# Optimization experiments

Measured on AMD Instinct MI355X. Metric: run time of the kernel, lower is better.

## Reference

```python
import jax, jax.numpy as jnp
import numpy as np

B, N, E, H, HID = 4, 2048, 1024, 16, 4096
D = E // H
EPS = 1e-5


def setup_inputs() -> dict:
    key = jax.random.key(0)
    ks = jax.random.split(key, 8)
    s = 0.02
    return {
        "x": jax.random.normal(ks[0], (B, N, E), dtype=jnp.float32),
        "Wqkv": jax.random.normal(ks[1], (3 * E, E), dtype=jnp.float32) * s,
        "bqkv": jnp.zeros((3 * E,), dtype=jnp.float32),
        "Wo": jax.random.normal(ks[2], (E, E), dtype=jnp.float32) * s,
        "bo": jnp.zeros((E,), dtype=jnp.float32),
        "ln1_g": jnp.ones((E,), dtype=jnp.float32),
        "ln1_b": jnp.zeros((E,), dtype=jnp.float32),
        "W1": jax.random.normal(ks[3], (HID, E), dtype=jnp.float32) * s,
        "bf1": jnp.zeros((HID,), dtype=jnp.float32),
        "W2": jax.random.normal(ks[4], (E, HID), dtype=jnp.float32) * s,
        "bf2": jnp.zeros((E,), dtype=jnp.float32),
        "ln2_g": jnp.ones((E,), dtype=jnp.float32),
        "ln2_b": jnp.zeros((E,), dtype=jnp.float32),
    }


def _layernorm(x, g, b):
    m = jnp.mean(x, axis=-1, keepdims=True)
    v = jnp.mean(jnp.square(x - m), axis=-1, keepdims=True)
    return (x - m) * jax.lax.rsqrt(v + EPS) * g + b


def reference(x, Wqkv, bqkv, Wo, bo, ln1_g, ln1_b, W1, bf1, W2, bf2, ln2_g, ln2_b):
    Bx, Nx, Ex = x.shape
    # --- MultiHeadSelfAttention (faithful to original, including its einsum-label quirk) ---
    qkv = x @ Wqkv.T + bqkv                                   # (B,N,3E)
    qkv = qkv.reshape(Bx, Nx, 3, H, D).transpose(2, 0, 3, 1, 4)  # (3,B,H,N,D)
    q, k, v = qkv[0], qkv[1], qkv[2]                          # each (B,H,N,D)
    # original torch labels: q/k interpreted as (n,q,h,d) -> energy (B,N,H,H)
    energy = jnp.einsum('nqhd,nkhd->nhqk', q, k)
    attention = jax.nn.softmax(energy / (Ex ** 0.5), axis=-1)  # softmax over heads axis
    out = jnp.einsum('nhql,nlhd->nqhd', attention, v).reshape(Bx, Nx, Ex)
    attn_out = out @ Wo.T + bo
    # --- residual + LN1 ---
    h = _layernorm(x + attn_out, ln1_g, ln1_b)
    # --- FFN (dropout is identity in eval) ---
    f = jax.nn.gelu(h @ W1.T + bf1, approximate=False) @ W2.T + bf2
    # --- residual + LN2 ---
    return _layernorm(h + f, ln2_g, ln2_b)
```

## Files before the change

### kernel.cpp

```cpp
#include <hip/hip_runtime.h>
#include <hip/hip_bf16.h>
#include <math.h>

typedef __hip_bfloat16 bf16;
typedef __bf16 bf8v __attribute__((ext_vector_type(8)));
typedef float f4v __attribute__((ext_vector_type(4)));

__device__ inline float gelu_act(float v) {
    return 0.5f * v * (1.f + erff(v * 0.70710678118654752f));
}

__device__ inline void gld16(const void* g, void* l) {
    __builtin_amdgcn_global_load_lds(
        (__attribute__((address_space(1))) void*)g,
        (__attribute__((address_space(3))) void*)l, 16, 0, 0);
}

__global__ __launch_bounds__(256)
void cast_f2b(const float* __restrict__ X, bf16* __restrict__ Y, long n)
{
    const long i = ((long)blockIdx.x * 256 + threadIdx.x) * 4;
    if (i + 3 < n) {
        const float4 v = *(const float4*)(X + i);
        Y[i + 0] = __float2bfloat16(v.x);
        Y[i + 1] = __float2bfloat16(v.y);
        Y[i + 2] = __float2bfloat16(v.z);
        Y[i + 3] = __float2bfloat16(v.w);
    }
}

template<int ACT, bool HASRES, typename CT, int K, int BN>
__global__ __launch_bounds__(512, 2)
void gemm256(const bf16* __restrict__ A, const bf16* __restrict__ W,
             const float* __restrict__ bias, const float* __restrict__ Rr,
             CT* __restrict__ C, int N)
{
    extern __shared__ __align__(16) unsigned short lds[];
    constexpr int NT   = K / 32;
    constexpr int NREP = BN / 64;
    constexpr int A_SH = 256 * 32;
    constexpr int SLOT = A_SH + BN * 32;

    const int o     = blockIdx.y * gridDim.x + blockIdx.x;
    const int local = o >> 3;
    const int bm = (o & 7) * 4 + (local & 3);
    const int bn = local >> 2;
    const long row0 = (long)bm * 256;
    const long col0 = (long)bn * BN;

    const int tid  = threadIdx.x;
    const int lane = tid & 63;
    const int wave = tid >> 6;
    const int wm = wave >> 2;
    const int wn = wave & 3;
    const int fr = lane & 15;
    const int ksw = (((lane >> 4) ^ ((lane >> 2) & 3)) << 3);

    const int srow = tid >> 2;
    const int csrc = (tid & 3) ^ ((srow >> 2) & 3);
    const unsigned short* gA = (const unsigned short*)A + (row0 + srow) * (long)K + csrc * 8;
    const unsigned short* gB = (const unsigned short*)W + (col0 + srow) * (long)K + csrc * 8;
    unsigned short* const wbase = lds + wave * 512;

    auto stage = [&](int t) {
        const long k0 = (long)t * 32;
        unsigned short* sl = wbase + (t & 3) * SLOT;
        gld16(gA + k0,                 sl);
        gld16(gA + 128 * (long)K + k0, sl + 4096);
        gld16(gB + k0,                 sl + A_SH);
        if constexpr (BN == 256)
            gld16(gB + 128 * (long)K + k0, sl + A_SH + 4096);
    };

    f4v acc[8][NREP];
#pragma unroll
    for (int i = 0; i < 8; ++i)
#pragma unroll
        for (int j = 0; j < NREP; ++j) acc[i][j] = {0.f, 0.f, 0.f, 0.f};

    stage(0); stage(1); stage(2);

#pragma unroll 4
    for (int t = 0; t < NT; ++t) {
        if constexpr (BN == 256) {
            if (t + 2 < NT)      asm volatile("s_waitcnt vmcnt(8)" ::: "memory");
            else if (t + 1 < NT) asm volatile("s_waitcnt vmcnt(4)" ::: "memory");
            else                 asm volatile("s_waitcnt vmcnt(0)" ::: "memory");
        } else {
            if (t + 2 < NT)      asm volatile("s_waitcnt vmcnt(6)" ::: "memory");
            else if (t + 1 < NT) asm volatile("s_waitcnt vmcnt(3)" ::: "memory");
            else                 asm volatile("s_waitcnt vmcnt(0)" ::: "memory");
        }
        __builtin_amdgcn_s_barrier();
        __builtin_amdgcn_sched_barrier(0);
        if (t + 3 < NT) stage(t + 3);

        const unsigned short* sA = lds + (t & 3) * SLOT;
        const unsigned short* sB = sA + A_SH;

        bf8v bfrag[NREP];
#pragma unroll
        for (int ni = 0; ni < NREP; ++ni)
            bfrag[ni] = *(const bf8v*)&sB[(wn * (NREP * 16) + ni * 16 + fr) * 32 + ksw];

#pragma unroll
        for (int ph = 0; ph < 2; ++ph) {
            bf8v afrag[4];
#pragma unroll
            for (int mi = 0; mi < 4; ++mi)
                afrag[mi] = *(const bf8v*)&sA[(wm * 128 + ph * 64 + mi * 16 + fr) * 32 + ksw];
            __builtin_amdgcn_s_setprio(1);
#pragma unroll
            for (int mi = 0; mi < 4; ++mi)
#pragma unroll
                for (int ni = 0; ni < NREP; ++ni)
                    acc[ph * 4 + mi][ni] = __builtin_amdgcn_mfma_f32_16x16x32_bf16(
                        afrag[mi], bfrag[ni], acc[ph * 4 + mi][ni], 0, 0, 0);
            __builtin_amdgcn_s_setprio(0);
        }
    }
    __builtin_amdgcn_sched_barrier(0);

    constexpr int STR = (BN == 256) ? 260 : 132;
    constexpr int LPR = BN / 4;
    constexpr int RPI = 64 / LPR;
    float* eb = (float*)lds;
    const int q4    = (lane >> 4) * 4;
    const int wrcol = wn * (NREP * 16) + fr;
    const int lcol  = (lane % LPR) * 4;
    const int lrow  = lane / LPR;
    const long nbase = col0 + lcol;
    const float4 b4 = *(const float4*)&bias[nbase];
    const float bb[4] = {b4.x, b4.y, b4.z, b4.w};

#pragma unroll
    for (int h = 0; h < 2; ++h) {
        __syncthreads();
        if (wm == h) {
#pragma unroll
            for (int mi = 0; mi < 8; ++mi)
#pragma unroll
                for (int ni = 0; ni < NREP; ++ni)
#pragma unroll
                    for (int r = 0; r < 4; ++r)
                        eb[(mi * 16 + q4 + r) * STR + wrcol + ni * 16] = acc[mi][ni][r];
        }
        __syncthreads();
#pragma unroll
        for (int i = 0; i < 16 / RPI; ++i) {
            const int  rh = wave * 16 + i * RPI + lrow;
            const long gr = row0 + h * 128 + rh;
            const f4v v = *(const f4v*)&eb[rh * STR + lcol];
            float ov[4];
#pragma unroll
            for (int c = 0; c < 4; ++c) ov[c] = v[c] + bb[c];
            if (HASRES) {
                const float4 r4 = *(const float4*)&Rr[gr * (long)N + nbase];
                const float ra[4] = {r4.x, r4.y, r4.z, r4.w};
#pragma unroll
                for (int c = 0; c < 4; ++c) ov[c] += ra[c];
            }
            if (ACT == 1) {
#pragma unroll
                for (int c = 0; c < 4; ++c) ov[c] = gelu_act(ov[c]);
            }
            if constexpr (sizeof(CT) == 2) {
                ushort4 s;
                bf16* sp = (bf16*)&s;
#pragma unroll
                for (int c = 0; c < 4; ++c) sp[c] = __float2bfloat16(ov[c]);
                *(ushort4*)&C[gr * (long)N + nbase] = s;
            } else {
                *(float4*)&C[gr * (long)N + nbase] = make_float4(ov[0], ov[1], ov[2], ov[3]);
            }
        }
    }
}

__global__ __launch_bounds__(256)
void attn_kernel(const bf16* __restrict__ qkv, bf16* __restrict__ scr)
{
    __shared__ float sb[4][3392];
    const int tid = threadIdx.x;
    const int wave = tid >> 6, lane = tid & 63;
    const int m = blockIdx.x * 4 + wave;

    float* q = sb[wave];
    float* k = q + 1040;
    float* v = k + 1040;
    float* a = v + 1040;

    const bf16* rowp = qkv + (size_t)m * 3072;
    for (int i = lane; i < 1024; i += 64) {
        int hh = i >> 6, dd = i & 63;
        q[hh * 65 + dd] = __bfloat162float(rowp[i]);
        k[hh * 65 + dd] = __bfloat162float(rowp[1024 + i]);
        v[hh * 65 + dd] = __bfloat162float(rowp[2048 + i]);
    }
    __syncthreads();

    const int h1 = lane & 15, qd = lane >> 4;
    float e[4];
#pragma unroll
    for (int j = 0; j < 4; ++j) {
        const float* qr = q + h1 * 65;
        const float* kr = k + (qd * 4 + j) * 65;
        float s0 = 0.f;
        for (int d = 0; d < 64; ++d) s0 += qr[d] * kr[d];
        e[j] = s0 * 0.03125f;
    }
    float mx = fmaxf(fmaxf(e[0], e[1]), fmaxf(e[2], e[3]));
    mx = fmaxf(mx, __shfl_xor(mx, 16, 64));
    mx = fmaxf(mx, __shfl_xor(mx, 32, 64));
    float p[4], ps = 0.f;
#pragma unroll
    for (int j = 0; j < 4; ++j) { p[j] = expf(e[j] - mx); ps += p[j]; }
    ps += __shfl_xor(ps, 16, 64);
    ps += __shfl_xor(ps, 32, 64);
    const float inv = 1.f / ps;
#pragma unroll
    for (int j = 0; j < 4; ++j) a[h1 * 17 + qd * 4 + j] = p[j] * inv;
    __syncthreads();

    const int h = lane & 15, dg = lane >> 4;
    float arow[16];
#pragma unroll
    for (int l2 = 0; l2 < 16; ++l2) arow[l2] = a[h * 17 + l2];
    const int b = m >> 11, j = m & 2047;
    bf16* op = scr + (((size_t)b * 2048 + h * 128 + (j >> 4)) * 1024 + (j & 15) * 64);
    for (int t = 0; t < 16; ++t) {
        const int d = dg * 16 + t;
        float o = 0.f;
#pragma unroll
        for (int l2 = 0; l2 < 16; ++l2) o += arow[l2] * v[l2 * 65 + d];
        op[d] = __float2bfloat16(o);
    }
}

__global__ __launch_bounds__(256)
void ln_kernel(const float* __restrict__ X, const float* __restrict__ G,
               const float* __restrict__ Bt, float* __restrict__ Y32,
               bf16* __restrict__ Yb)
{
    __shared__ float rs[4], rq[4];
    const int tid = threadIdx.x;
    const long row = blockIdx.x;
    const float* xp = X + row * 1024;
    float x[4];
#pragma unroll
    for (int i = 0; i < 4; ++i) x[i] = xp[tid + 256 * i];

    float s = x[0] + x[1] + x[2] + x[3];
#pragma unroll
    for (int off = 32; off; off >>= 1) s += __shfl_down(s, off, 64);
    if ((tid & 63) == 0) rs[tid >> 6] = s;
    __syncthreads();
    const float mean = (rs[0] + rs[1] + rs[2] + rs[3]) * (1.f / 1024.f);

    float qv = 0.f;
#pragma unroll
    for (int i = 0; i < 4; ++i) { float d = x[i] - mean; qv += d * d; }
#pragma unroll
    for (int off = 32; off; off >>= 1) qv += __shfl_down(qv, off, 64);
    if ((tid & 63) == 0) rq[tid >> 6] = qv;
    __syncthreads();
    const float var = (rq[0] + rq[1] + rq[2] + rq[3]) * (1.f / 1024.f);
    const float rstd = rsqrtf(var + 1e-5f);

#pragma unroll
    for (int i = 0; i < 4; ++i) {
        const int e = tid + 256 * i;
        const float yv = (x[i] - mean) * rstd * G[e] + Bt[e];
        Y32[row * 1024 + e] = yv;
        if (Yb) Yb[row * 1024 + e] = __float2bfloat16(yv);
    }
}

extern "C" void kernel_launch(void* const* d_in, const int* in_sizes, int n_in,
                              void* d_out, int out_size, void* d_ws, size_t ws_size,
                              hipStream_t stream)
{
    (void)in_sizes; (void)n_in; (void)out_size;
    const float* x    = (const float*)d_in[0];
    const float* Wqkv = (const float*)d_in[1];
    const float* bqkv = (const float*)d_in[2];
    const float* Wo   = (const float*)d_in[3];
    const float* bo   = (const float*)d_in[4];
    const float* g1   = (const float*)d_in[5];
    const float* b1   = (const float*)d_in[6];
    const float* W1   = (const float*)d_in[7];
    const float* bf1  = (const float*)d_in[8];
    const float* W2   = (const float*)d_in[9];
    const float* bf2  = (const float*)d_in[10];
    const float* g2   = (const float*)d_in[11];
    const float* b2   = (const float*)d_in[12];
    float* out = (float*)d_out;

    if (ws_size < 125829120ULL) return;

    char* ws = (char*)d_ws;
    bf16* qkv   = (bf16*)(ws + 0);
    float* t    = (float*)(ws + 0);
    bf16* u     = (bf16*)(ws + 0);
    bf16* Wqkvb = (bf16*)(ws + 67108864);
    bf16* Wob   = (bf16*)(ws + 73400320);
    bf16* W1b   = (bf16*)(ws + 75497472);
    bf16* W2b   = (bf16*)(ws + 83886080);
    bf16* xb    = (bf16*)(ws + 92274688);
    bf16* scr   = (bf16*)(ws + 92274688);
    bf16* hb    = (bf16*)(ws + 109051904);
    float* h    = out;

    constexpr unsigned LDS_BIG   = 133120;
    constexpr unsigned LDS_SMALL = 98304;

    cast_f2b<<<8192, 256, 0, stream>>>(x,    xb,    8388608);
    cast_f2b<<<3072, 256, 0, stream>>>(Wqkv, Wqkvb, 3145728);
    cast_f2b<<<1024, 256, 0, stream>>>(Wo,   Wob,   1048576);
    cast_f2b<<<4096, 256, 0, stream>>>(W1,   W1b,   4194304);
    cast_f2b<<<4096, 256, 0, stream>>>(W2,   W2b,   4194304);

    gemm256<0, false, bf16, 1024, 256><<<dim3(32, 12), 512, LDS_BIG, stream>>>(xb, Wqkvb, bqkv, nullptr, qkv, 3072);
    attn_kernel<<<2048, 256, 0, stream>>>(qkv, scr);
    gemm256<0, true, float, 1024, 128><<<dim3(32, 8), 512, LDS_SMALL, stream>>>(scr, Wob, bo, x, t, 1024);
    ln_kernel<<<8192, 256, 0, stream>>>(t, g1, b1, h, hb);
    gemm256<1, false, bf16, 1024, 256><<<dim3(32, 16), 512, LDS_BIG, stream>>>(hb, W1b, bf1, nullptr, u, 4096);
    gemm256<0, true, float, 4096, 128><<<dim3(32, 8), 512, LDS_SMALL, stream>>>(u, W2b, bf2, h, out, 1024);
    ln_kernel<<<8192, 256, 0, stream>>>(out, g2, b2, out, nullptr);
}
```

Baseline: 471.0 us.

## Interleave A/B tile prefetch with MFMA phases and change LDS swizzle

Restructures the GEMM main loop so the A-tile and B-tile global-to-LDS prefetches are issued separately, each interleaved with one of the two MFMA half-phases. Explicit barriers and lgkmcnt/vmcnt waits are added around each phase. The aim is to spread memory traffic evenly and overlap LDS fragment reads with compute. The LDS XOR swizzle also changes from (lane>>2)&3 to (lane>>1)&3 to reduce bank conflicts. The extra barriers per iteration add sync cost, and the new wait counts must match the split issue order.

```diff
diff --git a/kernel.cpp b/kernel.cpp
--- a/kernel.cpp
+++ b/kernel.cpp
@@ -54,19 +54,23 @@
     const int wm = wave >> 2;
     const int wn = wave & 3;
     const int fr = lane & 15;
-    const int ksw = (((lane >> 4) ^ ((lane >> 2) & 3)) << 3);
+    const int ksw = (((lane >> 4) ^ ((lane >> 1) & 3)) << 3);
 
     const int srow = tid >> 2;
-    const int csrc = (tid & 3) ^ ((srow >> 2) & 3);
+    const int csrc = (tid & 3) ^ ((srow >> 1) & 3);
     const unsigned short* gA = (const unsigned short*)A + (row0 + srow) * (long)K + csrc * 8;
     const unsigned short* gB = (const unsigned short*)W + (col0 + srow) * (long)K + csrc * 8;
     unsigned short* const wbase = lds + wave * 512;
 
-    auto stage = [&](int t) {
+    auto stageA = [&](int t) {
         const long k0 = (long)t * 32;
         unsigned short* sl = wbase + (t & 3) * SLOT;
         gld16(gA + k0,                 sl);
         gld16(gA + 128 * (long)K + k0, sl + 4096);
+    };
+    auto stageB = [&](int t) {
+        const long k0 = (long)t * 32;
+        unsigned short* sl = wbase + (t & 3) * SLOT;
         gld16(gB + k0,                 sl + A_SH);
         if constexpr (BN == 256)
             gld16(gB + 128 * (long)K + k0, sl + A_SH + 4096);
@@ -78,46 +82,64 @@
 #pragma unroll
         for (int j = 0; j < NREP; ++j) acc[i][j] = {0.f, 0.f, 0.f, 0.f};
 
-    stage(0); stage(1); stage(2);
+    stageA(0); stageB(0); stageA(1); stageB(1); stageA(2); stageB(2);
+    if constexpr (BN == 256) asm volatile("s_waitcnt vmcnt(8)" ::: "memory");
+    else                     asm volatile("s_waitcnt vmcnt(6)" ::: "memory");
+    __builtin_amdgcn_s_barrier();
 
 #pragma unroll 4
     for (int t = 0; t < NT; ++t) {
-        if constexpr (BN == 256) {
-            if (t + 2 < NT)      asm volatile("s_waitcnt vmcnt(8)" ::: "memory");
-            else if (t + 1 < NT) asm volatile("s_waitcnt vmcnt(4)" ::: "memory");
-            else                 asm volatile("s_waitcnt vmcnt(0)" ::: "memory");
-        } else {
-            if (t + 2 < NT)      asm volatile("s_waitcnt vmcnt(6)" ::: "memory");
-            else if (t + 1 < NT) asm volatile("s_waitcnt vmcnt(3)" ::: "memory");
-            else                 asm volatile("s_waitcnt vmcnt(0)" ::: "memory");
+        const unsigned short* sA = lds + (t & 3) * SLOT;
+        const unsigned short* sB = sA + A_SH;
+
+        bf8v bfrag[NREP], afrag[4];
+#pragma unroll
+        for (int ni = 0; ni < NREP; ++ni)
+            bfrag[ni] = *(const bf8v*)&sB[(wn * (NREP * 16) + ni * 16 + fr) * 32 + ksw];
+#pragma unroll
+        for (int mi = 0; mi < 4; ++mi)
+            afrag[mi] = *(const bf8v*)&sA[(wm * 128 + mi * 16 + fr) * 32 + ksw];
+        if (t + 3 < NT) stageA(t + 3);
+        __builtin_amdgcn_sched_barrier(0);
+        __builtin_amdgcn_s_barrier();
+        asm volatile("s_waitcnt lgkmcnt(0)" ::: "memory");
+        __builtin_amdgcn_sched_barrier(0);
+        __builtin_amdgcn_s_setprio(1);
+#pragma unroll
+        for (int mi = 0; mi < 4; ++mi)
+#pragma unroll
+            for (int ni = 0; ni < NREP; ++ni)
+                acc[mi][ni] = __builtin_amdgcn_mfma_f32_16x16x32_bf16(
+                    afrag[mi], bfrag[ni], acc[mi][ni], 0, 0, 0);
+        __builtin_amdgcn_s_setprio(0);
+        __builtin_amdgcn_s_barrier();
+
+#pragma unroll
+        for (int mi = 0; mi < 4; ++mi)
+            afrag[mi] = *(const bf8v*)&sA[(wm * 128 + 64 + mi * 16 + fr) * 32 + ksw];
+        if (t + 3 < NT) stageB(t + 3);
+        __builtin_amdgcn_sched_barrier(0);
+        if (t + 3 < NT) {
+            if constexpr (BN == 256) asm volatile("s_waitcnt vmcnt(8)" ::: "memory");
+            else                     asm volatile("s_waitcnt vmcnt(6)" ::: "memory");
+        } else if (t + 2 < NT) {
+            if constexpr (BN == 256) asm volatile("s_waitcnt vmcnt(4)" ::: "memory");
+            else                     asm volatile("s_waitcnt vmcnt(3)" ::: "memory");
+        } else if (t + 1 < NT) {
+            asm volatile("s_waitcnt vmcnt(0)" ::: "memory");
         }
         __builtin_amdgcn_s_barrier();
+        asm volatile("s_waitcnt lgkmcnt(0)" ::: "memory");
         __builtin_amdgcn_sched_barrier(0);
-        if (t + 3 < NT) stage(t + 3);
-
-        const unsigned short* sA = lds + (t & 3) * SLOT;
-        const unsigned short* sB = sA + A_SH;
-
-        bf8v bfrag[NREP];
-#pragma unroll
-        for (int ni = 0; ni < NREP; ++ni)
-            bfrag[ni] = *(const bf8v*)&sB[(wn * (NREP * 16) + ni * 16 + fr) * 32 + ksw];
-
-#pragma unroll
-        for (int ph = 0; ph < 2; ++ph) {
-            bf8v afrag[4];
-#pragma unroll
-            for (int mi = 0; mi < 4; ++mi)
-                afrag[mi] = *(const bf8v*)&sA[(wm * 128 + ph * 64 + mi * 16 + fr) * 32 + ksw];
-            __builtin_amdgcn_s_setprio(1);
-#pragma unroll
-            for (int mi = 0; mi < 4; ++mi)
-#pragma unroll
-                for (int ni = 0; ni < NREP; ++ni)
-                    acc[ph * 4 + mi][ni] = __builtin_amdgcn_mfma_f32_16x16x32_bf16(
-                        afrag[mi], bfrag[ni], acc[ph * 4 + mi][ni], 0, 0, 0);
-            __builtin_amdgcn_s_setprio(0);
-        }
+        __builtin_amdgcn_s_setprio(1);
+#pragma unroll
+        for (int mi = 0; mi < 4; ++mi)
+#pragma unroll
+            for (int ni = 0; ni < NREP; ++ni)
+                acc[4 + mi][ni] = __builtin_amdgcn_mfma_f32_16x16x32_bf16(
+                    afrag[mi], bfrag[ni], acc[4 + mi][ni], 0, 0, 0);
+        __builtin_amdgcn_s_setprio(0);
+        __builtin_amdgcn_s_barrier();
     }
     __builtin_amdgcn_sched_barrier(0);
 
```

Result: no change. 472.4 us (+0.3%).

## Replace 256-row GEMM with smaller 128x128 tile double-buffered kernel

Applied to the files above, without the earlier changes.

Replaces the 512-thread, 256xBN-tile GEMM, which used a 4-stage global_load_lds pipeline with explicit vmcnt waits and setprio, with a 256-thread 128x128-tile kernel. The new kernel uses 2-stage double buffering with __syncthreads and a simpler swizzle. Smaller tiles and LDS allow more workgroups per CU and more tiles in the grid, aiming at better occupancy and load balance. In exchange it gives up data reuse per tile and the deeper prefetch pipeline. Block-index remapping also changes to an XCD-strided scheme.

```diff
diff --git a/kernel.cpp b/kernel.cpp
--- a/kernel.cpp
+++ b/kernel.cpp
@@ -29,127 +29,104 @@
     }
 }
 
-template<int ACT, bool HASRES, typename CT, int K, int BN>
-__global__ __launch_bounds__(512, 2)
-void gemm256(const bf16* __restrict__ A, const bf16* __restrict__ W,
+template<int ACT, bool HASRES, typename CT, int K>
+__global__ __launch_bounds__(256, 4)
+void gemm128(const bf16* __restrict__ A, const bf16* __restrict__ W,
              const float* __restrict__ bias, const float* __restrict__ Rr,
              CT* __restrict__ C, int N)
 {
     extern __shared__ __align__(16) unsigned short lds[];
     constexpr int NT   = K / 32;
-    constexpr int NREP = BN / 64;
-    constexpr int A_SH = 256 * 32;
-    constexpr int SLOT = A_SH + BN * 32;
-
-    const int o     = blockIdx.y * gridDim.x + blockIdx.x;
-    const int local = o >> 3;
-    const int bm = (o & 7) * 4 + (local & 3);
-    const int bn = local >> 2;
-    const long row0 = (long)bm * 256;
-    const long col0 = (long)bn * BN;
+    constexpr int SLOT = 8192;
+
+    const int o   = blockIdx.y * gridDim.x + blockIdx.x;
+    const int nwg = gridDim.x * gridDim.y;
+    const int id  = (o & 7) * (nwg >> 3) + (o >> 3);
+    const int bm  = id % gridDim.x;
+    const int bn  = id / gridDim.x;
+    const long row0 = (long)bm * 128;
+    const long col0 = (long)bn * 128;
 
     const int tid  = threadIdx.x;
     const int lane = tid & 63;
     const int wave = tid >> 6;
-    const int wm = wave >> 2;
-    const int wn = wave & 3;
+    const int wm = wave >> 1;
+    const int wn = wave & 1;
     const int fr = lane & 15;
-    const int ksw = (((lane >> 4) ^ ((lane >> 2) & 3)) << 3);
+    const int ksw = (((lane >> 4) ^ ((lane >> 1) & 3)) << 3);
 
     const int srow = tid >> 2;
-    const int csrc = (tid & 3) ^ ((srow >> 2) & 3);
+    const int csrc = (tid & 3) ^ ((srow >> 1) & 3);
     const unsigned short* gA = (const unsigned short*)A + (row0 + srow) * (long)K + csrc * 8;
     const unsigned short* gB = (const unsigned short*)W + (col0 + srow) * (long)K + csrc * 8;
-    unsigned short* const wbase = lds + wave * 512;
+    const int woff = wave * 512;
 
     auto stage = [&](int t) {
         const long k0 = (long)t * 32;
-        unsigned short* sl = wbase + (t & 3) * SLOT;
+        unsigned short* sl = lds + (t & 1) * SLOT + woff;
         gld16(gA + k0,                 sl);
-        gld16(gA + 128 * (long)K + k0, sl + 4096);
-        gld16(gB + k0,                 sl + A_SH);
-        if constexpr (BN == 256)
-            gld16(gB + 128 * (long)K + k0, sl + A_SH + 4096);
+        gld16(gA + 64 * (long)K + k0,  sl + 2048);
+        gld16(gB + k0,                 sl + 4096);
+        gld16(gB + 64 * (long)K + k0,  sl + 6144);
     };
 
-    f4v acc[8][NREP];
-#pragma unroll
-    for (int i = 0; i < 8; ++i)
-#pragma unroll
-        for (int j = 0; j < NREP; ++j) acc[i][j] = {0.f, 0.f, 0.f, 0.f};
-
-    stage(0); stage(1); stage(2);
-
-#pragma unroll 4
+    f4v acc[4][4];
+#pragma unroll
+    for (int i = 0; i < 4; ++i)
+#pragma unroll
+        for (int j = 0; j < 4; ++j) acc[i][j] = {0.f, 0.f, 0.f, 0.f};
+
+    stage(0);
+    __syncthreads();
+
+#pragma unroll 2
     for (int t = 0; t < NT; ++t) {
-        if constexpr (BN == 256) {
-            if (t + 2 < NT)      asm volatile("s_waitcnt vmcnt(8)" ::: "memory");
-            else if (t + 1 < NT) asm volatile("s_waitcnt vmcnt(4)" ::: "memory");
-            else                 asm volatile("s_waitcnt vmcnt(0)" ::: "memory");
-        } else {
-            if (t + 2 < NT)      asm volatile("s_waitcnt vmcnt(6)" ::: "memory");
-            else if (t + 1 < NT) asm volatile("s_waitcnt vmcnt(3)" ::: "memory");
-            else                 asm volatile("s_waitcnt vmcnt(0)" ::: "memory");
+        if (t + 1 < NT) stage(t + 1);
+
+        const unsigned short* sA = lds + (t & 1) * SLOT;
+        const unsigned short* sB = sA + 4096;
+
+        bf8v afrag[4], bfrag[4];
+#pragma unroll
+        for (int x = 0; x < 4; ++x) {
+            afrag[x] = *(const bf8v*)&sA[(wm * 64 + x * 16 + fr) * 32 + ksw];
+            bfrag[x] = *(const bf8v*)&sB[(wn * 64 + x * 16 + fr) * 32 + ksw];
         }
-        __builtin_amdgcn_s_barrier();
-        __builtin_amdgcn_sched_barrier(0);
-        if (t + 3 < NT) stage(t + 3);
-
-        const unsigned short* sA = lds + (t & 3) * SLOT;
-        const unsigned short* sB = sA + A_SH;
-
-        bf8v bfrag[NREP];
-#pragma unroll
-        for (int ni = 0; ni < NREP; ++ni)
-            bfrag[ni] = *(const bf8v*)&sB[(wn * (NREP * 16) + ni * 16 + fr) * 32 + ksw];
-
-#pragma unroll
-        for (int ph = 0; ph < 2; ++ph) {
-            bf8v afrag[4];
-#pragma unroll
-            for (int mi = 0; mi < 4; ++mi)
-                afrag[mi] = *(const bf8v*)&sA[(wm * 128 + ph * 64 + mi * 16 + fr) * 32 + ksw];
-            __builtin_amdgcn_s_setprio(1);
-#pragma unroll
-            for (int mi = 0; mi < 4; ++mi)
-#pragma unroll
-                for (int ni = 0; ni < NREP; ++ni)
-                    acc[ph * 4 + mi][ni] = __builtin_amdgcn_mfma_f32_16x16x32_bf16(
-                        afrag[mi], bfrag[ni], acc[ph * 4 + mi][ni], 0, 0, 0);
-            __builtin_amdgcn_s_setprio(0);
-        }
-    }
-    __builtin_amdgcn_sched_barrier(0);
-
-    constexpr int STR = (BN == 256) ? 260 : 132;
-    constexpr int LPR = BN / 4;
-    constexpr int RPI = 64 / LPR;
+#pragma unroll
+        for (int mi = 0; mi < 4; ++mi)
+#pragma unroll
+            for (int ni = 0; ni < 4; ++ni)
+                acc[mi][ni] = __builtin_amdgcn_mfma_f32_16x16x32_bf16(
+                    afrag[mi], bfrag[ni], acc[mi][ni], 0, 0, 0);
+
+        __syncthreads();
+    }
+
+    constexpr int STR = 132;
     float* eb = (float*)lds;
     const int q4    = (lane >> 4) * 4;
-    const int wrcol = wn * (NREP * 16) + fr;
-    const int lcol  = (lane % LPR) * 4;
-    const int lrow  = lane / LPR;
+    const int lcol  = (tid & 31) * 4;
     const long nbase = col0 + lcol;
     const float4 b4 = *(const float4*)&bias[nbase];
     const float bb[4] = {b4.x, b4.y, b4.z, b4.w};
 
 #pragma unroll
     for (int h = 0; h < 2; ++h) {
-        __syncthreads();
+        if (h) __syncthreads();
         if (wm == h) {
 #pragma unroll
-            for (int mi = 0; mi < 8; ++mi)
-#pragma unroll
-                for (int ni = 0; ni < NREP; ++ni)
+            for (int mi = 0; mi < 4; ++mi)
+#pragma unroll
+                for (int ni = 0; ni < 4; ++ni)
 #pragma unroll
                     for (int r = 0; r < 4; ++r)
-                        eb[(mi * 16 + q4 + r) * STR + wrcol + ni * 16] = acc[mi][ni][r];
+                        eb[(mi * 16 + q4 + r) * STR + wn * 64 + ni * 16 + fr] = acc[mi][ni][r];
         }
         __syncthreads();
 #pragma unroll
-        for (int i = 0; i < 16 / RPI; ++i) {
-            const int  rh = wave * 16 + i * RPI + lrow;
-            const long gr = row0 + h * 128 + rh;
+        for (int i = 0; i < 8; ++i) {
+            const int  rh = i * 8 + (tid >> 5);
+            const long gr = row0 + h * 64 + rh;
             const f4v v = *(const f4v*)&eb[rh * STR + lcol];
             float ov[4];
 #pragma unroll
@@ -311,8 +288,7 @@
     bf16* hb    = (bf16*)(ws + 109051904);
     float* h    = out;
 
-    constexpr unsigned LDS_BIG   = 133120;
-    constexpr unsigned LDS_SMALL = 98304;
+    constexpr unsigned LDS_SZ = 33792;
 
     cast_f2b<<<8192, 256, 0, stream>>>(x,    xb,    8388608);
     cast_f2b<<<3072, 256, 0, stream>>>(Wqkv, Wqkvb, 3145728);
@@ -320,11 +296,11 @@
     cast_f2b<<<4096, 256, 0, stream>>>(W1,   W1b,   4194304);
     cast_f2b<<<4096, 256, 0, stream>>>(W2,   W2b,   4194304);
 
-    gemm256<0, false, bf16, 1024, 256><<<dim3(32, 12), 512, LDS_BIG, stream>>>(xb, Wqkvb, bqkv, nullptr, qkv, 3072);
+    gemm128<0, false, bf16, 1024><<<dim3(64, 24), 256, LDS_SZ, stream>>>(xb, Wqkvb, bqkv, nullptr, qkv, 3072);
     attn_kernel<<<2048, 256, 0, stream>>>(qkv, scr);
-    gemm256<0, true, float, 1024, 128><<<dim3(32, 8), 512, LDS_SMALL, stream>>>(scr, Wob, bo, x, t, 1024);
+    gemm128<0, true, float, 1024><<<dim3(64, 8), 256, LDS_SZ, stream>>>(scr, Wob, bo, x, t, 1024);
     ln_kernel<<<8192, 256, 0, stream>>>(t, g1, b1, h, hb);
-    gemm256<1, false, bf16, 1024, 256><<<dim3(32, 16), 512, LDS_BIG, stream>>>(hb, W1b, bf1, nullptr, u, 4096);
-    gemm256<0, true, float, 4096, 128><<<dim3(32, 8), 512, LDS_SMALL, stream>>>(u, W2b, bf2, h, out, 1024);
+    gemm128<1, false, bf16, 1024><<<dim3(64, 32), 256, LDS_SZ, stream>>>(hb, W1b, bf1, nullptr, u, 4096);
+    gemm128<0, true, float, 4096><<<dim3(64, 8), 256, LDS_SZ, stream>>>(u, W2b, bf2, h, out, 1024);
     ln_kernel<<<8192, 256, 0, stream>>>(out, g2, b2, out, nullptr);
 }
```

Measured after the change: 499.0 us. +6.0%, slower.
